# Performance work log

Measured on AMD Instinct MI355X. Metric: run time of the kernel, lower is better.

The kernel has to match this reference:

```python
import jax, jax.numpy as jnp
import numpy as np

B, S, D = 4, 2048, 1024
E = 8
H = int(D * 2.5)  # 2560


def setup_inputs() -> dict:
    key = jax.random.key(0)
    ks = jax.random.split(key, 6)
    scale = 0.02
    x = jax.random.normal(ks[0], (B, S, D), dtype=jnp.float32)
    Wr = jax.random.normal(ks[1], (E, D), dtype=jnp.float32) * scale   # router: logits = x @ Wr.T
    Wg = jax.random.normal(ks[2], (E, H, D), dtype=jnp.float32) * scale  # gate proj per expert
    Wu = jax.random.normal(ks[3], (E, H, D), dtype=jnp.float32) * scale  # up proj per expert
    Wd = jax.random.normal(ks[4], (E, D, H), dtype=jnp.float32) * scale  # down proj per expert
    return {"x": x, "Wr": Wr, "Wg": Wg, "Wu": Wu, "Wd": Wd, "top_k": 2}


def reference(x, Wr, Wg, Wu, Wd, top_k):
    num_experts = Wg.shape[0]
    logits = jnp.einsum('bsd,ed->bse', x, Wr)              # [B,S,E]
    probs = jax.nn.softmax(logits, axis=-1)
    k = min(top_k, num_experts)
    topv, topi = jax.lax.top_k(probs, k)                   # [B,S,k]
    out = jnp.zeros_like(x)
    for ei in range(num_experts):
        mask = jnp.any(topi == ei, axis=-1)                # [B,S] bool
        h = jax.nn.silu(jnp.einsum('bsd,hd->bsh', x, Wg[ei])) \
            * jnp.einsum('bsd,hd->bsh', x, Wu[ei])         # [B,S,H]
        ex = jnp.einsum('bsh,dh->bsd', h, Wd[ei])          # [B,S,D]
        w = (probs[..., ei] * mask.astype(x.dtype))[..., None]
        out = out + ex * w
    return (out, logits, probs, topi)
```

## Files before the change

### kernel.cpp

```cpp
#include <hip/hip_runtime.h>

#define T_TOK 8192
#define DD    1024
#define EE    8
#define HH    2560
#define PAIR_CAP (T_TOK*2 + 128)
#define MT_MAX 64
#define NT1   (HH/64)
#define NT2   (DD/128)

typedef __attribute__((ext_vector_type(8))) short bf16x8;
typedef __attribute__((ext_vector_type(4))) float f32x4;

__device__ __forceinline__ unsigned short f2b(float f) {
  union { float f; unsigned u; } v; v.f = f;
  unsigned r = v.u + 0x7FFFu + ((v.u >> 16) & 1u);
  return (unsigned short)(r >> 16);
}

__device__ __forceinline__ void async16(const void* g, void* l) {
  __builtin_amdgcn_global_load_lds(
      (const __attribute__((address_space(1))) unsigned int*)(unsigned long long)g,
      (__attribute__((address_space(3))) unsigned int*)l,
      16, 0, 0);
}

__global__ void zero_ints(int* a, int n) {
  int i = threadIdx.x;
  if (i < n) a[i] = 0;
}

__global__ void conv_bf16_3(const float* __restrict__ s0, const float* __restrict__ s1,
                            const float* __restrict__ s2,
                            unsigned short* __restrict__ d0, unsigned short* __restrict__ d1,
                            unsigned short* __restrict__ d2, int n4) {
  int i = blockIdx.x * blockDim.x + threadIdx.x;
  if (i >= n4) return;
  const float* s = (blockIdx.y == 0) ? s0 : (blockIdx.y == 1) ? s1 : s2;
  unsigned short* d = (blockIdx.y == 0) ? d0 : (blockIdx.y == 1) ? d1 : d2;
  float4 v = ((const float4*)s)[i];
  ushort4 o;
  o.x = f2b(v.x); o.y = f2b(v.y); o.z = f2b(v.z); o.w = f2b(v.w);
  ((ushort4*)d)[i] = o;
}

__global__ __launch_bounds__(256) void router(
    const float* __restrict__ x, const float* __restrict__ Wr,
    unsigned short* __restrict__ xb,
    float* __restrict__ o_logits, float* __restrict__ o_probs, float* __restrict__ o_topi,
    int* __restrict__ top_e, float* __restrict__ top_p, int* __restrict__ counts)
{
  __shared__ float sWr[EE * DD];
  int tid = threadIdx.x;
  const float4* w4 = (const float4*)Wr;
  float4* s4 = (float4*)sWr;
  for (int i = tid; i < EE * DD / 4; i += 256) s4[i] = w4[i];
  __syncthreads();

  int wv = tid >> 6, lane = tid & 63;
  int t = blockIdx.x * 4 + wv;
  const float4* xt4 = (const float4*)(x + (size_t)t * DD);
  ushort4* xbt = (ushort4*)(xb + (size_t)t * DD);

  float acc[EE];
#pragma unroll
  for (int e = 0; e < EE; e++) acc[e] = 0.f;
#pragma unroll
  for (int p = 0; p < 4; p++) {
    float4 v = xt4[p * 64 + lane];
    ushort4 o;
    o.x = f2b(v.x); o.y = f2b(v.y); o.z = f2b(v.z); o.w = f2b(v.w);
    xbt[p * 64 + lane] = o;
    int d = (p * 64 + lane) * 4;
#pragma unroll
    for (int e = 0; e < EE; e++) {
      const float* wr = &sWr[e * DD + d];
      acc[e] += v.x * wr[0] + v.y * wr[1] + v.z * wr[2] + v.w * wr[3];
    }
  }
#pragma unroll
  for (int e = 0; e < EE; e++) {
#pragma unroll
    for (int off = 32; off; off >>= 1) acc[e] += __shfl_down(acc[e], off);
  }
  if (lane == 0) {
    float mx = acc[0];
#pragma unroll
    for (int e = 1; e < EE; e++) mx = fmaxf(mx, acc[e]);
    float p[EE]; float sum = 0.f;
#pragma unroll
    for (int e = 0; e < EE; e++) { p[e] = __expf(acc[e] - mx); sum += p[e]; }
    float inv = 1.f / sum;
#pragma unroll
    for (int e = 0; e < EE; e++) {
      p[e] *= inv;
      o_logits[(size_t)t * EE + e] = acc[e];
      o_probs [(size_t)t * EE + e] = p[e];
    }
    int i0 = 0;
#pragma unroll
    for (int e = 1; e < EE; e++) if (p[e] > p[i0]) i0 = e;
    int i1 = (i0 == 0) ? 1 : 0;
#pragma unroll
    for (int e = 0; e < EE; e++) if (e != i0 && p[e] > p[i1]) i1 = e;

    o_topi[t * 2 + 0] = (float)i0;
    o_topi[t * 2 + 1] = (float)i1;
    top_e[t * 2 + 0] = i0; top_e[t * 2 + 1] = i1;
    top_p[t * 2 + 0] = p[i0]; top_p[t * 2 + 1] = p[i1];
    atomicAdd(&counts[i0], 1);
    atomicAdd(&counts[i1], 1);
  }
}

__global__ void mk_offsets(const int* __restrict__ counts, int* __restrict__ offsets,
                           int* __restrict__ cursors) {
  if (threadIdx.x == 0) {
    int s = 0;
    for (int e = 0; e < EE; e++) { offsets[e] = s; s += counts[e]; }
  }
  if (threadIdx.x < EE) cursors[threadIdx.x] = 0;
}

__global__ void scatter(const int* __restrict__ top_e,
                        const int* __restrict__ offsets, int* __restrict__ cursors,
                        int* __restrict__ list, int* __restrict__ slot) {
  int t = blockIdx.x * blockDim.x + threadIdx.x;
  if (t >= T_TOK) return;
#pragma unroll
  for (int k = 0; k < 2; k++) {
    int e = top_e[t * 2 + k];
    int pos = atomicAdd(&cursors[e], 1);
    int dst = offsets[e] + pos;
    list[dst] = t;
    slot[t * 2 + k] = dst;
  }
}

__global__ __launch_bounds__(256) void gemm_gateup(
    const unsigned short* __restrict__ xb,
    const unsigned short* __restrict__ Wgb,
    const unsigned short* __restrict__ Wub,
    const int* __restrict__ list, const int* __restrict__ offsets,
    const int* __restrict__ counts,
    unsigned short* __restrict__ hbuf)
{
  int bx = blockIdx.x;
  int e = bx / (MT_MAX * NT1);
  int rem = bx - e * (MT_MAX * NT1);
  int mt = rem / NT1;
  int nt = rem - mt * NT1;
  int n_e = counts[e];
  if (mt * 128 >= n_e) return;
  int off_e = offsets[e];

  __shared__ unsigned short sA [2][128 * 32];
  __shared__ unsigned short sBg[2][ 64 * 32];
  __shared__ unsigned short sBu[2][ 64 * 32];

  int tid = threadIdx.x, wv = tid >> 6, lane = tid & 63;
  const unsigned short* wg_e = Wgb + (size_t)e * HH * DD;
  const unsigned short* wu_e = Wub + (size_t)e * HH * DD;

  size_t aBase[2];
#pragma unroll
  for (int i = 0; i < 2; i++) {
    int c = i * 256 + tid;
    int r = c >> 2, j = c & 3;
    int jj = j ^ ((r >> 1) & 3);
    int idx = mt * 128 + r;
    if (idx >= n_e) idx = n_e - 1;
    int tok = list[off_e + idx];
    aBase[i] = (size_t)tok * DD + (size_t)(jj * 8);
  }
  size_t bBase;
  {
    int r = tid >> 2, j = tid & 3;
    int jj = j ^ ((r >> 1) & 3);
    bBase = (size_t)(nt * 64 + r) * DD + (size_t)(jj * 8);
  }

  f32x4 accg[4][2] = {};
  f32x4 accu[4][2] = {};
  int wm = (wv >> 1) * 64, wn = (wv & 1) * 32;

  auto stage = [&](int b, int k0) {
    async16(xb  + aBase[0] + k0, &sA [b][(      wv * 64) * 8]);
    async16(xb  + aBase[1] + k0, &sA [b][(256 + wv * 64) * 8]);
    async16(wg_e + bBase   + k0, &sBg[b][(      wv * 64) * 8]);
    async16(wu_e + bBase   + k0, &sBu[b][(      wv * 64) * 8]);
  };

  const int NK = DD / 32;
  stage(0, 0);
  stage(1, 32);
  int q = lane >> 4;
  for (int t = 0; t < NK; ++t) {
    int cur = t & 1;
    if (t == NK - 1) asm volatile("s_waitcnt vmcnt(0)" ::: "memory");
    else             asm volatile("s_waitcnt vmcnt(4)" ::: "memory");
    __builtin_amdgcn_s_barrier();

    bf16x8 af[4], bg[2], bu[2];
#pragma unroll
    for (int fi = 0; fi < 4; fi++) {
      int r = wm + fi * 16 + (lane & 15);
      int ch = q ^ ((r >> 1) & 3);
      af[fi] = *(const bf16x8*)&sA[cur][r * 32 + ch * 8];
    }
#pragma unroll
    for (int fj = 0; fj < 2; fj++) {
      int r = wn + fj * 16 + (lane & 15);
      int ch = q ^ ((r >> 1) & 3);
      bg[fj] = *(const bf16x8*)&sBg[cur][r * 32 + ch * 8];
      bu[fj] = *(const bf16x8*)&sBu[cur][r * 32 + ch * 8];
    }
    asm volatile("s_waitcnt lgkmcnt(0)" ::: "memory");
    __builtin_amdgcn_sched_barrier(0);
    __builtin_amdgcn_s_barrier();
    if (t + 2 < NK) stage(cur, (t + 2) * 32);

    __builtin_amdgcn_s_setprio(1);
#pragma unroll
    for (int fi = 0; fi < 4; fi++)
#pragma unroll
      for (int fj = 0; fj < 2; fj++) {
        accg[fi][fj] = __builtin_amdgcn_mfma_f32_16x16x32_bf16(af[fi], bg[fj], accg[fi][fj], 0, 0, 0);
        accu[fi][fj] = __builtin_amdgcn_mfma_f32_16x16x32_bf16(af[fi], bu[fj], accu[fi][fj], 0, 0, 0);
      }
    __builtin_amdgcn_s_setprio(0);
  }

#pragma unroll
  for (int fi = 0; fi < 4; fi++) {
    int mBase = mt * 128 + wm + fi * 16 + ((lane >> 4) << 2);
#pragma unroll
    for (int fj = 0; fj < 2; fj++) {
      int col = nt * 64 + wn + fj * 16 + (lane & 15);
#pragma unroll
      for (int r = 0; r < 4; r++) {
        int m = mBase + r;
        if (m < n_e) {
          float g = accg[fi][fj][r];
          float u = accu[fi][fj][r];
          float hv = g / (1.f + __expf(-g)) * u;
          hbuf[(size_t)(off_e + m) * HH + col] = f2b(hv);
        }
      }
    }
  }
}

__global__ __launch_bounds__(256) void gemm_down(
    const unsigned short* __restrict__ hbuf,
    const unsigned short* __restrict__ Wdb,
    const int* __restrict__ offsets,
    const int* __restrict__ counts,
    float* __restrict__ tmp)
{
  int bx = blockIdx.x;
  int e = bx / (MT_MAX * NT2);
  int rem = bx - e * (MT_MAX * NT2);
  int mt = rem / NT2;
  int nt = rem - mt * NT2;
  int n_e = counts[e];
  if (mt * 128 >= n_e) return;
  int off_e = offsets[e];

  __shared__ unsigned short sA[2][128 * 32];
  __shared__ unsigned short sB[2][128 * 32];
  int tid = threadIdx.x, wv = tid >> 6, lane = tid & 63;
  const unsigned short* wd_e = Wdb + (size_t)e * DD * HH;

  size_t aBase[2], bBase[2];
#pragma unroll
  for (int i = 0; i < 2; i++) {
    int c = i * 256 + tid;
    int r = c >> 2, j = c & 3;
    int jj = j ^ ((r >> 1) & 3);
    aBase[i] = (size_t)(off_e + mt * 128 + r) * HH + (size_t)(jj * 8);
    bBase[i] = (size_t)(nt * 128 + r) * HH + (size_t)(jj * 8);
  }

  f32x4 acc[4][4] = {};
  int wm = (wv >> 1) * 64, wn = (wv & 1) * 64;

  auto stage = [&](int b, int k0) {
    async16(hbuf + aBase[0] + k0, &sA[b][(      wv * 64) * 8]);
    async16(hbuf + aBase[1] + k0, &sA[b][(256 + wv * 64) * 8]);
    async16(wd_e + bBase[0] + k0, &sB[b][(      wv * 64) * 8]);
    async16(wd_e + bBase[1] + k0, &sB[b][(256 + wv * 64) * 8]);
  };

  const int NK = HH / 32;
  stage(0, 0);
  stage(1, 32);
  int q = lane >> 4;
  for (int t = 0; t < NK; ++t) {
    int cur = t & 1;
    if (t == NK - 1) asm volatile("s_waitcnt vmcnt(0)" ::: "memory");
    else             asm volatile("s_waitcnt vmcnt(4)" ::: "memory");
    __builtin_amdgcn_s_barrier();

    bf16x8 af[4], bfr[4];
#pragma unroll
    for (int f = 0; f < 4; f++) {
      int ra = wm + f * 16 + (lane & 15);
      int ca = q ^ ((ra >> 1) & 3);
      af[f] = *(const bf16x8*)&sA[cur][ra * 32 + ca * 8];
      int rb = wn + f * 16 + (lane & 15);
      int cb = q ^ ((rb >> 1) & 3);
      bfr[f] = *(const bf16x8*)&sB[cur][rb * 32 + cb * 8];
    }
    asm volatile("s_waitcnt lgkmcnt(0)" ::: "memory");
    __builtin_amdgcn_sched_barrier(0);
    __builtin_amdgcn_s_barrier();
    if (t + 2 < NK) stage(cur, (t + 2) * 32);

    __builtin_amdgcn_s_setprio(1);
#pragma unroll
    for (int fi = 0; fi < 4; fi++)
#pragma unroll
      for (int fj = 0; fj < 4; fj++)
        acc[fi][fj] = __builtin_amdgcn_mfma_f32_16x16x32_bf16(af[fi], bfr[fj], acc[fi][fj], 0, 0, 0);
    __builtin_amdgcn_s_setprio(0);
  }

#pragma unroll
  for (int fi = 0; fi < 4; fi++) {
    int mBase = mt * 128 + wm + fi * 16 + ((lane >> 4) << 2);
#pragma unroll
    for (int r = 0; r < 4; r++) {
      int m = mBase + r;
      if (m < n_e) {
        float* orow = tmp + (size_t)(off_e + m) * DD + nt * 128 + wn;
#pragma unroll
        for (int fj = 0; fj < 4; fj++)
          orow[fj * 16 + (lane & 15)] = acc[fi][fj][r];
      }
    }
  }
}

__global__ __launch_bounds__(256) void combine(
    const float* __restrict__ tmp, const int* __restrict__ slot,
    const float* __restrict__ top_p, float* __restrict__ out)
{
  int t = blockIdx.x, d = threadIdx.x;
  int s0 = slot[t * 2 + 0], s1 = slot[t * 2 + 1];
  float p0 = top_p[t * 2 + 0], p1 = top_p[t * 2 + 1];
  float4 a = ((const float4*)(tmp + (size_t)s0 * DD))[d];
  float4 b = ((const float4*)(tmp + (size_t)s1 * DD))[d];
  float4 o;
  o.x = p0 * a.x + p1 * b.x;
  o.y = p0 * a.y + p1 * b.y;
  o.z = p0 * a.z + p1 * b.z;
  o.w = p0 * a.w + p1 * b.w;
  ((float4*)(out + (size_t)t * DD))[d] = o;
}

extern "C" void kernel_launch(void* const* d_in, const int* in_sizes, int n_in,
                              void* d_out, int out_size, void* d_ws, size_t ws_size,
                              hipStream_t stream) {
  const float* x  = (const float*)d_in[0];
  const float* Wr = (const float*)d_in[1];
  const float* Wg = (const float*)d_in[2];
  const float* Wu = (const float*)d_in[3];
  const float* Wd = (const float*)d_in[4];

  float* out      = (float*)d_out;
  float* o_logits = out + (size_t)T_TOK * DD;
  float* o_probs  = o_logits + (size_t)T_TOK * EE;
  float* o_topi   = o_probs + (size_t)T_TOK * EE;

  char* w = (char*)d_ws;
  auto alloc = [&](size_t bytes) {
    char* p = w;
    w += (bytes + 255) & ~(size_t)255;
    return p;
  };
  unsigned short* Wgb = (unsigned short*)alloc((size_t)EE * HH * DD * 2);
  unsigned short* Wub = (unsigned short*)alloc((size_t)EE * HH * DD * 2);
  unsigned short* Wdb = (unsigned short*)alloc((size_t)EE * DD * HH * 2);
  unsigned short* xb  = (unsigned short*)alloc((size_t)T_TOK * DD * 2);
  unsigned short* hb  = (unsigned short*)alloc((size_t)PAIR_CAP * HH * 2);
  int*   top_e   = (int*)  alloc((size_t)T_TOK * 2 * 4);
  float* top_p   = (float*)alloc((size_t)T_TOK * 2 * 4);
  int*   counts  = (int*)  alloc(64);
  int*   offsets = (int*)  alloc(64);
  int*   cursors = (int*)  alloc(64);
  int*   list    = (int*)  alloc((size_t)PAIR_CAP * 4);
  int*   slot    = (int*)  alloc((size_t)T_TOK * 2 * 4);

  float* tmp = (float*)Wgb;

  zero_ints<<<1, 64, 0, stream>>>(counts, EE);
  {
    int nw4 = EE * HH * DD / 4;
    dim3 g((nw4 + 255) / 256, 3);
    conv_bf16_3<<<g, 256, 0, stream>>>(Wg, Wu, Wd, Wgb, Wub, Wdb, nw4);
  }
  router<<<T_TOK / 4, 256, 0, stream>>>(x, Wr, xb, o_logits, o_probs, o_topi, top_e, top_p, counts);
  mk_offsets<<<1, 64, 0, stream>>>(counts, offsets, cursors);
  scatter<<<T_TOK / 256, 256, 0, stream>>>(top_e, offsets, cursors, list, slot);
  gemm_gateup<<<EE * MT_MAX * NT1, 256, 0, stream>>>(xb, Wgb, Wub, list, offsets, counts, hb);
  gemm_down<<<EE * MT_MAX * NT2, 256, 0, stream>>>(hb, Wdb, offsets, counts, tmp);
  combine<<<T_TOK, 256, 0, stream>>>(tmp, slot, top_p, out);
}
```

Before: 899.4 us.

## Fold counter zeroing into conversion, aggregate scatter atomics, unroll GEMM K loops

Removes the separate zero_ints launch by zeroing the expert counters inside the weight-conversion kernel. The scatter kernel now aggregates its per-expert atomics per wavefront with ballot/popcount and one atomicAdd per expert group. Both GEMM main loops are unrolled by two over the double buffer, with precomputed byte offsets for the LDS and global addresses and a peeled tail, to cut per-iteration index arithmetic. Costs are more code and register pressure, and the slot order within each expert changes.

```diff
diff --git a/kernel.cpp b/kernel.cpp
--- a/kernel.cpp
+++ b/kernel.cpp
@@ -25,15 +25,11 @@
       16, 0, 0);
 }
 
-__global__ void zero_ints(int* a, int n) {
-  int i = threadIdx.x;
-  if (i < n) a[i] = 0;
-}
-
 __global__ void conv_bf16_3(const float* __restrict__ s0, const float* __restrict__ s1,
                             const float* __restrict__ s2,
                             unsigned short* __restrict__ d0, unsigned short* __restrict__ d1,
-                            unsigned short* __restrict__ d2, int n4) {
+                            unsigned short* __restrict__ d2, int n4, int* __restrict__ counts) {
+  if (blockIdx.x == 0 && blockIdx.y == 0 && threadIdx.x < EE) counts[threadIdx.x] = 0;
   int i = blockIdx.x * blockDim.x + threadIdx.x;
   if (i >= n4) return;
   const float* s = (blockIdx.y == 0) ? s0 : (blockIdx.y == 1) ? s1 : s2;
@@ -127,10 +123,24 @@
                         int* __restrict__ list, int* __restrict__ slot) {
   int t = blockIdx.x * blockDim.x + threadIdx.x;
   if (t >= T_TOK) return;
+  int lane = threadIdx.x & 63;
+  unsigned long long lower = (lane == 63) ? ~0ull >> 1 : (1ull << lane) - 1;
 #pragma unroll
   for (int k = 0; k < 2; k++) {
     int e = top_e[t * 2 + k];
-    int pos = atomicAdd(&cursors[e], 1);
+    int pos = 0;
+#pragma unroll
+    for (int ee = 0; ee < EE; ee++) {
+      unsigned long long m = __ballot(e == ee);
+      if (e == ee) {
+        int rank = __popcll(m & lower);
+        int base = 0;
+        if (rank == 0) base = atomicAdd(&cursors[ee], __popcll(m));
+        int src = __ffsll((long long)m) - 1;
+        base = __shfl(base, src);
+        pos = base + rank;
+      }
+    }
     int dst = offsets[e] + pos;
     list[dst] = t;
     slot[t * 2 + k] = dst;
@@ -179,48 +189,88 @@
     int jj = j ^ ((r >> 1) & 3);
     bBase = (size_t)(nt * 64 + r) * DD + (size_t)(jj * 8);
   }
+  const char* pA0 = (const char*)(xb + aBase[0]);
+  const char* pA1 = (const char*)(xb + aBase[1]);
+  const char* pBg = (const char*)(wg_e + bBase);
+  const char* pBu = (const char*)(wu_e + bBase);
 
   f32x4 accg[4][2] = {};
   f32x4 accu[4][2] = {};
   int wm = (wv >> 1) * 64, wn = (wv & 1) * 32;
-
-  auto stage = [&](int b, int k0) {
-    async16(xb  + aBase[0] + k0, &sA [b][(      wv * 64) * 8]);
-    async16(xb  + aBase[1] + k0, &sA [b][(256 + wv * 64) * 8]);
-    async16(wg_e + bBase   + k0, &sBg[b][(      wv * 64) * 8]);
-    async16(wu_e + bBase   + k0, &sBu[b][(      wv * 64) * 8]);
+  int q = lane >> 4;
+
+  int offA[4], offB[2];
+#pragma unroll
+  for (int f = 0; f < 4; f++) {
+    int r = wm + f * 16 + (lane & 15);
+    int ch = q ^ ((r >> 1) & 3);
+    offA[f] = r * 64 + ch * 16;
+  }
+#pragma unroll
+  for (int f = 0; f < 2; f++) {
+    int r = wn + f * 16 + (lane & 15);
+    int ch = q ^ ((r >> 1) & 3);
+    offB[f] = r * 64 + ch * 16;
+  }
+  const char* cA  = (const char*)sA;
+  const char* cBg = (const char*)sBg;
+  const char* cBu = (const char*)sBu;
+
+  auto stage = [&](int b, int kb) {
+    async16(pA0 + kb, &sA [b][(      wv * 64) * 8]);
+    async16(pA1 + kb, &sA [b][(256 + wv * 64) * 8]);
+    async16(pBg + kb, &sBg[b][(      wv * 64) * 8]);
+    async16(pBu + kb, &sBu[b][(      wv * 64) * 8]);
   };
 
   const int NK = DD / 32;
   stage(0, 0);
-  stage(1, 32);
-  int q = lane >> 4;
-  for (int t = 0; t < NK; ++t) {
-    int cur = t & 1;
-    if (t == NK - 1) asm volatile("s_waitcnt vmcnt(0)" ::: "memory");
-    else             asm volatile("s_waitcnt vmcnt(4)" ::: "memory");
+  stage(1, 64);
+  int kpre = 128;
+  for (int t = 0; t < NK - 2; t += 2) {
+#pragma unroll
+    for (int half = 0; half < 2; half++) {
+      asm volatile("s_waitcnt vmcnt(4)" ::: "memory");
+      __builtin_amdgcn_s_barrier();
+      bf16x8 af[4], bg[2], bu[2];
+#pragma unroll
+      for (int f = 0; f < 4; f++) af[f] = *(const bf16x8*)(cA + half * 8192 + offA[f]);
+#pragma unroll
+      for (int f = 0; f < 2; f++) {
+        bg[f] = *(const bf16x8*)(cBg + half * 4096 + offB[f]);
+        bu[f] = *(const bf16x8*)(cBu + half * 4096 + offB[f]);
+      }
+      asm volatile("s_waitcnt lgkmcnt(0)" ::: "memory");
+      __builtin_amdgcn_sched_barrier(0);
+      __builtin_amdgcn_s_barrier();
+      stage(half, kpre);
+      kpre += 64;
+      __builtin_amdgcn_s_setprio(1);
+#pragma unroll
+      for (int fi = 0; fi < 4; fi++)
+#pragma unroll
+        for (int fj = 0; fj < 2; fj++) {
+          accg[fi][fj] = __builtin_amdgcn_mfma_f32_16x16x32_bf16(af[fi], bg[fj], accg[fi][fj], 0, 0, 0);
+          accu[fi][fj] = __builtin_amdgcn_mfma_f32_16x16x32_bf16(af[fi], bu[fj], accu[fi][fj], 0, 0, 0);
+        }
+      __builtin_amdgcn_s_setprio(0);
+    }
+  }
+#pragma unroll
+  for (int half = 0; half < 2; half++) {
+    if (half == 0) asm volatile("s_waitcnt vmcnt(4)" ::: "memory");
+    else           asm volatile("s_waitcnt vmcnt(0)" ::: "memory");
     __builtin_amdgcn_s_barrier();
-
     bf16x8 af[4], bg[2], bu[2];
 #pragma unroll
-    for (int fi = 0; fi < 4; fi++) {
-      int r = wm + fi * 16 + (lane & 15);
-      int ch = q ^ ((r >> 1) & 3);
-      af[fi] = *(const bf16x8*)&sA[cur][r * 32 + ch * 8];
-    }
-#pragma unroll
-    for (int fj = 0; fj < 2; fj++) {
-      int r = wn + fj * 16 + (lane & 15);
-      int ch = q ^ ((r >> 1) & 3);
-      bg[fj] = *(const bf16x8*)&sBg[cur][r * 32 + ch * 8];
-      bu[fj] = *(const bf16x8*)&sBu[cur][r * 32 + ch * 8];
+    for (int f = 0; f < 4; f++) af[f] = *(const bf16x8*)(cA + half * 8192 + offA[f]);
+#pragma unroll
+    for (int f = 0; f < 2; f++) {
+      bg[f] = *(const bf16x8*)(cBg + half * 4096 + offB[f]);
+      bu[f] = *(const bf16x8*)(cBu + half * 4096 + offB[f]);
     }
     asm volatile("s_waitcnt lgkmcnt(0)" ::: "memory");
     __builtin_amdgcn_sched_barrier(0);
-    __builtin_amdgcn_s_barrier();
-    if (t + 2 < NK) stage(cur, (t + 2) * 32);
-
-    __builtin_amdgcn_s_setprio(1);
 #pragma unroll
     for (int fi = 0; fi < 4; fi++)
 #pragma unroll
@@ -228,7 +278,6 @@
         accg[fi][fj] = __builtin_amdgcn_mfma_f32_16x16x32_bf16(af[fi], bg[fj], accg[fi][fj], 0, 0, 0);
         accu[fi][fj] = __builtin_amdgcn_mfma_f32_16x16x32_bf16(af[fi], bu[fj], accu[fi][fj], 0, 0, 0);
       }
-    __builtin_amdgcn_s_setprio(0);
   }
 
 #pragma unroll
@@ -281,49 +330,82 @@
     aBase[i] = (size_t)(off_e + mt * 128 + r) * HH + (size_t)(jj * 8);
     bBase[i] = (size_t)(nt * 128 + r) * HH + (size_t)(jj * 8);
   }
+  const char* pA0 = (const char*)(hbuf + aBase[0]);
+  const char* pA1 = (const char*)(hbuf + aBase[1]);
+  const char* pB0 = (const char*)(wd_e + bBase[0]);
+  const char* pB1 = (const char*)(wd_e + bBase[1]);
 
   f32x4 acc[4][4] = {};
   int wm = (wv >> 1) * 64, wn = (wv & 1) * 64;
-
-  auto stage = [&](int b, int k0) {
-    async16(hbuf + aBase[0] + k0, &sA[b][(      wv * 64) * 8]);
-    async16(hbuf + aBase[1] + k0, &sA[b][(256 + wv * 64) * 8]);
-    async16(wd_e + bBase[0] + k0, &sB[b][(      wv * 64) * 8]);
-    async16(wd_e + bBase[1] + k0, &sB[b][(256 + wv * 64) * 8]);
+  int q = lane >> 4;
+
+  int offA[4], offB[4];
+#pragma unroll
+  for (int f = 0; f < 4; f++) {
+    int ra = wm + f * 16 + (lane & 15);
+    int ca = q ^ ((ra >> 1) & 3);
+    offA[f] = ra * 64 + ca * 16;
+    int rb = wn + f * 16 + (lane & 15);
+    int cb = q ^ ((rb >> 1) & 3);
+    offB[f] = rb * 64 + cb * 16;
+  }
+  const char* cA = (const char*)sA;
+  const char* cB = (const char*)sB;
+
+  auto stage = [&](int b, int kb) {
+    async16(pA0 + kb, &sA[b][(      wv * 64) * 8]);
+    async16(pA1 + kb, &sA[b][(256 + wv * 64) * 8]);
+    async16(pB0 + kb, &sB[b][(      wv * 64) * 8]);
+    async16(pB1 + kb, &sB[b][(256 + wv * 64) * 8]);
   };
 
   const int NK = HH / 32;
   stage(0, 0);
-  stage(1, 32);
-  int q = lane >> 4;
-  for (int t = 0; t < NK; ++t) {
-    int cur = t & 1;
-    if (t == NK - 1) asm volatile("s_waitcnt vmcnt(0)" ::: "memory");
-    else             asm volatile("s_waitcnt vmcnt(4)" ::: "memory");
+  stage(1, 64);
+  int kpre = 128;
+  for (int t = 0; t < NK - 2; t += 2) {
+#pragma unroll
+    for (int half = 0; half < 2; half++) {
+      asm volatile("s_waitcnt vmcnt(4)" ::: "memory");
+      __builtin_amdgcn_s_barrier();
+      bf16x8 af[4], bfr[4];
+#pragma unroll
+      for (int f = 0; f < 4; f++) {
+        af[f]  = *(const bf16x8*)(cA + half * 8192 + offA[f]);
+        bfr[f] = *(const bf16x8*)(cB + half * 8192 + offB[f]);
+      }
+      asm volatile("s_waitcnt lgkmcnt(0)" ::: "memory");
+      __builtin_amdgcn_sched_barrier(0);
+      __builtin_amdgcn_s_barrier();
+      stage(half, kpre);
+      kpre += 64;
+      __builtin_amdgcn_s_setprio(1);
+#pragma unroll
+      for (int fi = 0; fi < 4; fi++)
+#pragma unroll
+        for (int fj = 0; fj < 4; fj++)
+          acc[fi][fj] = __builtin_amdgcn_mfma_f32_16x16x32_bf16(af[fi], bfr[fj], acc[fi][fj], 0, 0, 0);
+      __builtin_amdgcn_s_setprio(0);
+    }
+  }
+#pragma unroll
+  for (int half = 0; half < 2; half++) {
+    if (half == 0) asm volatile("s_waitcnt vmcnt(4)" ::: "memory");
+    else           asm volatile("s_waitcnt vmcnt(0)" ::: "memory");
     __builtin_amdgcn_s_barrier();
-
     bf16x8 af[4], bfr[4];
 #pragma unroll
     for (int f = 0; f < 4; f++) {
-      int ra = wm + f * 16 + (lane & 15);
-      int ca = q ^ ((ra >> 1) & 3);
-      af[f] = *(const bf16x8*)&sA[cur][ra * 32 + ca * 8];
-      int rb = wn + f * 16 + (lane & 15);
-      int cb = q ^ ((rb >> 1) & 3);
-      bfr[f] = *(const bf16x8*)&sB[cur][rb * 32 + cb * 8];
+      af[f]  = *(const bf16x8*)(cA + half * 8192 + offA[f]);
+      bfr[f] = *(const bf16x8*)(cB + half * 8192 + offB[f]);
     }
     asm volatile("s_waitcnt lgkmcnt(0)" ::: "memory");
     __builtin_amdgcn_sched_barrier(0);
-    __builtin_amdgcn_s_barrier();
-    if (t + 2 < NK) stage(cur, (t + 2) * 32);
-
-    __builtin_amdgcn_s_setprio(1);
 #pragma unroll
     for (int fi = 0; fi < 4; fi++)
 #pragma unroll
       for (int fj = 0; fj < 4; fj++)
         acc[fi][fj] = __builtin_amdgcn_mfma_f32_16x16x32_bf16(af[fi], bfr[fj], acc[fi][fj], 0, 0, 0);
-    __builtin_amdgcn_s_setprio(0);
   }
 
 #pragma unroll
@@ -394,11 +476,10 @@
 
   float* tmp = (float*)Wgb;
 
-  zero_ints<<<1, 64, 0, stream>>>(counts, EE);
   {
     int nw4 = EE * HH * DD / 4;
     dim3 g((nw4 + 255) / 256, 3);
-    conv_bf16_3<<<g, 256, 0, stream>>>(Wg, Wu, Wd, Wgb, Wub, Wdb, nw4);
+    conv_bf16_3<<<g, 256, 0, stream>>>(Wg, Wu, Wd, Wgb, Wub, Wdb, nw4, counts);
   }
   router<<<T_TOK / 4, 256, 0, stream>>>(x, Wr, xb, o_logits, o_probs, o_topi, top_e, top_p, counts);
   mk_offsets<<<1, 64, 0, stream>>>(counts, offsets, cursors);
```

New measurement: 903.2 us. Within noise of the previous version (+0.4%).
